# Optimization experiments

Hardware: AMD Instinct MI355X
Metric: run time of the kernel (lower is better)

## Reference

```python
import jax, jax.numpy as jnp
import numpy as np

B=8; C=2; H=256; W=64; PH=4; PW=4; HP=H//PH; WP=W//PW; N=HP*WP
HID=1024; NH=16; HD=HID//NH; DEPTH=8; FFN=int(int(HID*4)*2/3); TDIM=256; OUT=PH*PW*C
EPS=1e-6


def _rmsnorm(x, w):
    return x * jax.lax.rsqrt(jnp.mean(x*x, -1, keepdims=True) + EPS) * w


def _modulate(x, shift, scale):
    return x * (1.0 + scale[:, None, :]) + shift[:, None, :]


def _rotate_half(x):
    x1 = x[..., 0::2]
    x2 = x[..., 1::2]
    return jnp.stack([-x2, x1], axis=-1).reshape(x.shape)


def _rope_tables():
    # 2D axial RoPE (EVA VisionRotaryEmbeddingFast style), dim per axis = HD//2
    dim = HD // 2
    freqs = 1.0 / (10000.0 ** (np.arange(0, dim, 2, dtype=np.float32) / dim))
    fh = np.repeat(np.outer(np.arange(HP, dtype=np.float32), freqs), 2, axis=-1)  # [HP,dim]
    fw = np.repeat(np.outer(np.arange(WP, dtype=np.float32), freqs), 2, axis=-1)  # [WP,dim]
    f = np.concatenate([np.broadcast_to(fh[:, None, :], (HP, WP, dim)),
                        np.broadcast_to(fw[None, :, :], (HP, WP, dim))], -1).reshape(N, HD)
    return jnp.asarray(np.cos(f)), jnp.asarray(np.sin(f))


def _sincos_1d(dim, pos):
    omega = np.arange(dim // 2, dtype=np.float32) / (dim / 2.0)
    omega = 1.0 / 10000.0 ** omega
    out = np.einsum('n,d->nd', pos.reshape(-1).astype(np.float32), omega)
    return np.concatenate([np.sin(out), np.cos(out)], -1)


def _pos_embed():
    gw, gh = np.meshgrid(np.arange(WP), np.arange(HP))  # row-major (HP, WP) grids
    emb = np.concatenate([_sincos_1d(HID // 2, gw), _sincos_1d(HID // 2, gh)], -1)
    return jnp.asarray(emb, dtype=jnp.float32)  # [N, HID]


_COS, _SIN = _rope_tables()
_POS = _pos_embed()


def _timestep_emb(t):
    half = TDIM // 2
    freqs = jnp.exp(-jnp.log(jnp.float32(10000.0)) * jnp.arange(half, dtype=jnp.float32) / half)
    args = t[:, None] * freqs[None]
    return jnp.concatenate([jnp.cos(args), jnp.sin(args)], -1)


def setup_inputs() -> dict:
    key = jax.random.key(0)
    ks = iter(jax.random.split(key, 16))
    def w(shape, s=0.02):
        return jax.random.normal(next(ks), shape, dtype=jnp.float32) * s
    return {
        'x': jax.random.normal(next(ks), (B, C, H, W), dtype=jnp.float32),
        't': jax.random.uniform(next(ks), (B,), dtype=jnp.float32) * 1000.0,
        'patch_w': w((HID, C, PH, PW)), 'patch_b': jnp.zeros((HID,), jnp.float32),
        't_w': w((HID, TDIM)), 't_b': jnp.zeros((HID,), jnp.float32),
        'norm1_w': jnp.ones((DEPTH, HID), jnp.float32),
        'qkv_w': w((DEPTH, 3 * HID, HID)), 'qkv_b': jnp.zeros((DEPTH, 3 * HID), jnp.float32),
        'qn_w': jnp.ones((DEPTH, HD), jnp.float32), 'kn_w': jnp.ones((DEPTH, HD), jnp.float32),
        'proj_w': w((DEPTH, HID, HID)), 'proj_b': jnp.zeros((DEPTH, HID), jnp.float32),
        'norm2_w': jnp.ones((DEPTH, HID), jnp.float32),
        'w12_w': w((DEPTH, 2 * FFN, HID)), 'w12_b': jnp.zeros((DEPTH, 2 * FFN), jnp.float32),
        'w3_w': w((DEPTH, HID, FFN)), 'w3_b': jnp.zeros((DEPTH, HID), jnp.float32),
        'ada_w': w((DEPTH, 6 * HID, HID)), 'ada_b': jnp.zeros((DEPTH, 6 * HID), jnp.float32),
        'fnorm_w': jnp.ones((HID,), jnp.float32),
        'flin_w': w((OUT, HID)), 'flin_b': jnp.zeros((OUT,), jnp.float32),
        'fada_w': w((2 * HID, HID)), 'fada_b': jnp.zeros((2 * HID,), jnp.float32),
    }


def reference(x, t, patch_w, patch_b, t_w, t_b, norm1_w, qkv_w, qkv_b, qn_w, kn_w,
              proj_w, proj_b, norm2_w, w12_w, w12_b, w3_w, w3_b, ada_w, ada_b,
              fnorm_w, flin_w, flin_b, fada_w, fada_b):
    # timestep embedding -> c : [B, HID]
    c = _timestep_emb(t) @ t_w.T + t_b
    cs = jax.nn.silu(c)
    # patch embed (conv stride==kernel == patchify + matmul)
    xp = x.reshape(B, C, HP, PH, WP, PW)
    h = jnp.einsum('bchpwq,ocpq->bhwo', xp, patch_w).reshape(B, N, HID) + patch_b
    h = h + _POS[None]
    scale = 1.0 / np.sqrt(HD)
    for d in range(DEPTH):
        ada = cs @ ada_w[d].T + ada_b[d]
        sm, scm, gm, sp, scp, gp = jnp.split(ada, 6, axis=-1)
        hn = _modulate(_rmsnorm(h, norm1_w[d]), sm, scm)
        qkv = (hn @ qkv_w[d].T + qkv_b[d]).reshape(B, N, 3, NH, HD).transpose(2, 0, 3, 1, 4)
        q, k, v = qkv[0], qkv[1], qkv[2]  # [B, NH, N, HD]
        q = _rmsnorm(q, qn_w[d]) 
        k = _rmsnorm(k, kn_w[d])
        q = q * _COS + _rotate_half(q) * _SIN
        k = k * _COS + _rotate_half(k) * _SIN
        attn = jax.nn.softmax(jnp.einsum('bhqd,bhkd->bhqk', q, k) * scale, axis=-1)
        o = jnp.einsum('bhqk,bhkd->bqhd', attn, v).reshape(B, N, HID)
        o = o @ proj_w[d].T + proj_b[d]
        h = h + gm[:, None, :] * o
        hn = _modulate(_rmsnorm(h, norm2_w[d]), sp, scp)
        x12 = hn @ w12_w[d].T + w12_b[d]
        x1, x2 = jnp.split(x12, 2, axis=-1)
        h = h + gp[:, None, :] * ((jax.nn.silu(x1) * x2) @ w3_w[d].T + w3_b[d])
    fsh, fsc = jnp.split(cs @ fada_w.T + fada_b, 2, axis=-1)
    h = _modulate(_rmsnorm(h, fnorm_w), fsh, fsc) @ flin_w.T + flin_b  # [B, N, OUT]
    y = h.reshape(B, HP, WP, PH, PW, C)
    return jnp.einsum('nhwpqc->nchpwq', y).reshape(B, C, H, W)
```

## Files before the change

kernel.cpp:

```cpp
#include <hip/hip_runtime.h>
#include <stdint.h>

typedef __bf16 bf16;
typedef __attribute__((ext_vector_type(8))) __bf16 bf16x8;
typedef __attribute__((ext_vector_type(4))) float floatx4;

#define NTOK   1024
#define TOKS   8192
#define HID_   1024
#define FFN_   2730
#define FFNP   2816
#define X12N   5460

#define EPI_BF16  0
#define EPI_QKV   1
#define EPI_RESID 2

__global__ __launch_bounds__(256) void conv_bf16(const float* __restrict__ in, bf16* __restrict__ out, int n)
{
    const int i = (blockIdx.x * 256 + threadIdx.x) * 4;
    if (i >= n) return;
    const float4 v = *(const float4*)(in + i);
    out[i + 0] = (bf16)v.x; out[i + 1] = (bf16)v.y;
    out[i + 2] = (bf16)v.z; out[i + 3] = (bf16)v.w;
}

__global__ void conv_pad_w3(const float* __restrict__ w3, bf16* __restrict__ w3p)
{
    const int kk = blockIdx.x * 256 + threadIdx.x;
    const int row = blockIdx.y;
    if (kk >= FFNP) return;
    w3p[(size_t)row * FFNP + kk] = (kk < FFN_) ? (bf16)w3[(size_t)row * FFN_ + kk] : (bf16)0.f;
}

#define GLL(src, dst) __builtin_amdgcn_global_load_lds( \
    (const __attribute__((address_space(1))) void*)(src), \
    (__attribute__((address_space(3))) void*)(dst), 16, 0, 0)

#define STAGE_A(bufi, hi, tile) GLL(pA[hi] + (size_t)(tile) * 64, As + (bufi) * 16384 + ((hi) * 512 + t) * 8)
#define STAGE_B(bufi, hi, tile) GLL(pB[hi] + (size_t)(tile) * 64, Bs + (bufi) * 16384 + ((hi) * 512 + t) * 8)

#define LOADA(bufi, qm) { _Pragma("unroll") for (int mf = 0; mf < 4; mf++) { \
    a[mf][0] = *(const bf16x8*)(As + (bufi) * 16384 + (qm) * 8192 + arow64 + mf * 1024 + swz0); \
    a[mf][1] = *(const bf16x8*)(As + (bufi) * 16384 + (qm) * 8192 + arow64 + mf * 1024 + swz1); } }

#define LOADB(bufi, qn) { _Pragma("unroll") for (int nf = 0; nf < 2; nf++) { \
    b[nf][0] = *(const bf16x8*)(Bs + (bufi) * 16384 + (qn) * 8192 + brow64 + nf * 1024 + swz0); \
    b[nf][1] = *(const bf16x8*)(Bs + (bufi) * 16384 + (qn) * 8192 + brow64 + nf * 1024 + swz1); } }

#define MM(qm, qn) { _Pragma("unroll") for (int mf = 0; mf < 4; mf++) \
    _Pragma("unroll") for (int nf = 0; nf < 2; nf++) { \
    acc[qm][qn][mf][nf] = __builtin_amdgcn_mfma_f32_16x16x32_bf16(a[mf][0], b[nf][0], acc[qm][qn][mf][nf], 0, 0, 0); \
    acc[qm][qn][mf][nf] = __builtin_amdgcn_mfma_f32_16x16x32_bf16(a[mf][1], b[nf][1], acc[qm][qn][mf][nf], 0, 0, 0); } }

#define PHTAIL(...) { __builtin_amdgcn_s_barrier(); \
    asm volatile("s_waitcnt lgkmcnt(0)" ::: "memory"); \
    __builtin_amdgcn_sched_barrier(0); \
    __builtin_amdgcn_s_setprio(1); __VA_ARGS__; __builtin_amdgcn_s_setprio(0); \
    __builtin_amdgcn_s_barrier(); }

__global__ __launch_bounds__(512, 2) void gemm256(
    const bf16* __restrict__ A, const bf16* __restrict__ Bm, const float* __restrict__ bias,
    int K, int Nreal, int epi,
    bf16* __restrict__ outb, int ldo,
    bf16* __restrict__ qo, bf16* __restrict__ ko, bf16* __restrict__ vo,
    float* __restrict__ hres, const float* __restrict__ gate, int gstride)
{
    __shared__ __align__(16) bf16 As[2 * 16384];
    __shared__ __align__(16) bf16 Bs[2 * 16384];
    const int t = threadIdx.x;

    const int gx = gridDim.x;
    int wg = blockIdx.y * gx + blockIdx.x;
    {
        const int nwg = gx * gridDim.y;
        const int q8 = nwg >> 3, r8 = nwg & 7;
        const int xcd = wg & 7, pos = wg >> 3;
        wg = (xcd < r8 ? xcd * (q8 + 1) : r8 * (q8 + 1) + (xcd - r8) * q8) + pos;
    }
    const int M0 = (wg / gx) * 256, N0 = (wg % gx) * 256;
    const int Nlast = Nreal - 1;

    const int lane = t & 63, w = t >> 6;
    const int wm = w >> 2, wn = w & 3;
    const int quad = lane >> 4, r16 = lane & 15;

    const int rS = t >> 3;
    const int cswS = (t & 7) ^ (rS & 7);
    const bf16* pA[4]; const bf16* pB[4];
    #pragma unroll
    for (int hi = 0; hi < 4; hi++) {
        pA[hi] = A + (size_t)(M0 + hi * 64 + rS) * K + cswS * 8;
        int nb = N0 + hi * 64 + rS; if (nb > Nlast) nb = Nlast;
        pB[hi] = Bm + (size_t)nb * K + cswS * 8;
    }

    const int arow64 = (wm * 64 + r16) * 64;
    const int brow64 = (wn * 32 + r16) * 64;
    const int swz0 = ((0 * 4 + quad) ^ (r16 & 7)) * 8;
    const int swz1 = ((1 * 4 + quad) ^ (r16 & 7)) * 8;

    floatx4 acc[2][2][4][2];
    const floatx4 zero = {0.f, 0.f, 0.f, 0.f};
    #pragma unroll
    for (int i0 = 0; i0 < 2; i0++)
        #pragma unroll
        for (int i1 = 0; i1 < 2; i1++)
            #pragma unroll
            for (int i2 = 0; i2 < 4; i2++)
                #pragma unroll
                for (int i3 = 0; i3 < 2; i3++) acc[i0][i1][i2][i3] = zero;
    bf16x8 a[4][2], b[2][2];

    const int NT = K >> 6;
    const int NI = NT >> 1;

    STAGE_A(0, 0, 0); STAGE_A(0, 1, 0);
    STAGE_B(0, 0, 0); STAGE_B(0, 1, 0);
    STAGE_B(0, 2, 0); STAGE_B(0, 3, 0);
    STAGE_A(0, 2, 0); STAGE_A(0, 3, 0);
    STAGE_A(1, 0, 1); STAGE_A(1, 1, 1);
    STAGE_B(1, 0, 1); STAGE_B(1, 1, 1);
    asm volatile("s_waitcnt vmcnt(4)" ::: "memory");
    __builtin_amdgcn_s_barrier();

    for (int it = 0; it < NI; ++it) {
        const bool last = (it == NI - 1);
        const int to = 2 * it + 1, te2 = 2 * it + 2, to2 = 2 * it + 3;
        LOADA(0, 0); LOADB(0, 0);
        STAGE_A(1, 2, to); STAGE_A(1, 3, to);
        PHTAIL(MM(0, 0));
        LOADB(0, 1);
        STAGE_B(1, 2, to); STAGE_B(1, 3, to);
        PHTAIL(MM(0, 1));
        LOADA(0, 1); LOADB(0, 0);
        if (!last) { STAGE_A(0, 0, te2); STAGE_A(0, 1, te2); }
        PHTAIL(MM(1, 0));
        LOADB(0, 1);
        if (!last) { STAGE_B(0, 0, te2); STAGE_B(0, 1, te2);
                     asm volatile("s_waitcnt vmcnt(4)" ::: "memory"); }
        else       { asm volatile("s_waitcnt vmcnt(0)" ::: "memory"); }
        PHTAIL(MM(1, 1));
        LOADA(1, 0); LOADB(1, 0);
        if (!last) { STAGE_A(0, 2, te2); STAGE_A(0, 3, te2); }
        PHTAIL(MM(0, 0));
        LOADB(1, 1);
        if (!last) { STAGE_B(0, 2, te2); STAGE_B(0, 3, te2); }
        PHTAIL(MM(0, 1));
        LOADA(1, 1); LOADB(1, 0);
        if (!last) { STAGE_A(1, 0, to2); STAGE_A(1, 1, to2); }
        PHTAIL(MM(1, 0));
        LOADB(1, 1);
        if (!last) { STAGE_B(1, 0, to2); STAGE_B(1, 1, to2);
                     asm volatile("s_waitcnt vmcnt(4)" ::: "memory"); }
        PHTAIL(MM(1, 1));
    }

    #pragma unroll
    for (int qm = 0; qm < 2; qm++)
    #pragma unroll
    for (int mf = 0; mf < 4; mf++) {
        const int rbase = M0 + qm * 128 + wm * 64 + mf * 16 + quad * 4;
        #pragma unroll
        for (int qn = 0; qn < 2; qn++)
        #pragma unroll
        for (int nf = 0; nf < 2; nf++) {
            const int col = N0 + qn * 128 + wn * 32 + nf * 16 + r16;
            if (col >= Nreal) continue;
            const float bv = bias[col];
            const floatx4 av = acc[qm][qn][mf][nf];
            if (epi == EPI_BF16) {
                #pragma unroll
                for (int rr = 0; rr < 4; rr++)
                    outb[(size_t)(rbase + rr) * ldo + col] = (bf16)(av[rr] + bv);
            } else if (epi == EPI_QKV) {
                const int s = col >> 10, hh = (col >> 6) & 15, dd = col & 63;
                #pragma unroll
                for (int rr = 0; rr < 4; rr++) {
                    const int row = rbase + rr;
                    const int bb = row >> 10, n = row & 1023;
                    const float vv = av[rr] + bv;
                    if (s == 0)      qo[((size_t)(bb * 16 + hh) * 1024 + n) * 64 + dd] = (bf16)vv;
                    else if (s == 1) ko[((size_t)(bb * 16 + hh) * 1024 + n) * 64 + dd] = (bf16)vv;
                    else             vo[((size_t)(bb * 16 + hh) * 64 + dd) * 1024 + n] = (bf16)vv;
                }
            } else {
                #pragma unroll
                for (int rr = 0; rr < 4; rr++) {
                    const int row = rbase + rr;
                    const int bb = row >> 10;
                    hres[(size_t)row * 1024 + col] += gate[(size_t)bb * gstride + col] * (av[rr] + bv);
                }
            }
        }
    }
}

__global__ __launch_bounds__(256) void small_gemm(
    const float* __restrict__ Aws, const float* __restrict__ t_in,
    const float* __restrict__ W, const float* __restrict__ bias,
    float* __restrict__ out, int N, int K, int mode, int dosilu)
{
    const int w = threadIdx.x >> 6, lane = threadIdx.x & 63;
    const int col = blockIdx.x * 4 + w;
    float acc[8];
    #pragma unroll
    for (int bb = 0; bb < 8; bb++) acc[bb] = 0.f;
    float tb[8];
    if (mode == 1) {
        #pragma unroll
        for (int bb = 0; bb < 8; bb++) tb[bb] = t_in[bb];
    }
    for (int kk = lane; kk < K; kk += 64) {
        const float wv = W[(size_t)col * K + kk];
        if (mode == 1) {
            const float f = __expf(-(float)(kk & 127) * (9.21034037198f / 128.f));
            #pragma unroll
            for (int bb = 0; bb < 8; bb++) {
                const float arg = tb[bb] * f;
                const float e = (kk < 128) ? cosf(arg) : sinf(arg);
                acc[bb] += e * wv;
            }
        } else {
            #pragma unroll
            for (int bb = 0; bb < 8; bb++) acc[bb] += Aws[(size_t)bb * 1024 + kk] * wv;
        }
    }
    #pragma unroll
    for (int bb = 0; bb < 8; bb++) {
        float v2 = acc[bb];
        #pragma unroll
        for (int off = 32; off; off >>= 1) v2 += __shfl_xor(v2, off, 64);
        acc[bb] = v2;
    }
    if (lane == 0) {
        const float bv = bias[col];
        #pragma unroll
        for (int bb = 0; bb < 8; bb++) {
            float vv = acc[bb] + bv;
            if (dosilu) vv = vv / (1.f + __expf(-vv));
            out[(size_t)bb * N + col] = vv;
        }
    }
}

__global__ __launch_bounds__(256) void patch_embed(
    const float* __restrict__ x, const float* __restrict__ pw, const float* __restrict__ pb,
    float* __restrict__ h)
{
    __shared__ float xs[32];
    const int row = blockIdx.x, t = threadIdx.x;
    const int b = row >> 10, n = row & 1023;
    const int hp = n >> 4, wp = n & 15;
    if (t < 32) {
        const int c = t >> 4, ph = (t >> 2) & 3, pq = t & 3;
        xs[t] = x[((size_t)(b * 2 + c) * 256 + hp * 4 + ph) * 64 + wp * 4 + pq];
    }
    __syncthreads();
    #pragma unroll
    for (int rep = 0; rep < 4; rep++) {
        const int o = t + rep * 256;
        const float* wrow = pw + (size_t)o * 32;
        float acc = pb[o];
        #pragma unroll
        for (int e = 0; e < 32; e++) acc += xs[e] * wrow[e];
        const int seg = o >> 8, oo = o & 255;
        const float om = __expf(-(float)oo * (9.21034037198f / 256.f));
        const float pos = (seg < 2) ? (float)wp : (float)hp;
        const float arg = pos * om;
        const float pe = ((seg & 1) == 0) ? sinf(arg) : cosf(arg);
        h[(size_t)row * 1024 + o] = acc + pe;
    }
}

__global__ __launch_bounds__(256) void norm_mod(
    const float* __restrict__ h, const float* __restrict__ w,
    const float* __restrict__ ada, int sh_off, int sc_off, int stride,
    bf16* __restrict__ out)
{
    __shared__ float red[4];
    const int row = blockIdx.x, t = threadIdx.x;
    const int b = row >> 10;
    const float4 xv = ((const float4*)(h + (size_t)row * 1024))[t];
    float ss = xv.x * xv.x + xv.y * xv.y + xv.z * xv.z + xv.w * xv.w;
    #pragma unroll
    for (int off = 32; off; off >>= 1) ss += __shfl_xor(ss, off, 64);
    if ((t & 63) == 0) red[t >> 6] = ss;
    __syncthreads();
    const float total = red[0] + red[1] + red[2] + red[3];
    const float rms = rsqrtf(total * (1.f / 1024.f) + 1e-6f);
    const float* sh = ada + (size_t)b * stride + sh_off;
    const float* sc = ada + (size_t)b * stride + sc_off;
    const float vals[4] = {xv.x, xv.y, xv.z, xv.w};
    #pragma unroll
    for (int e = 0; e < 4; e++) {
        const int c2 = t * 4 + e;
        const float vv = vals[e] * rms * w[c2] * (1.f + sc[c2]) + sh[c2];
        out[(size_t)row * 1024 + c2] = (bf16)vv;
    }
}

__global__ __launch_bounds__(256) void rope_qk(
    bf16* __restrict__ q, bf16* __restrict__ k,
    const float* __restrict__ qw, const float* __restrict__ kw)
{
    const int n = blockIdx.x * 4 + (threadIdx.x >> 6);
    const int bh = blockIdx.y, d = threadIdx.x & 63;
    const size_t idx = ((size_t)bh * 1024 + n) * 64 + d;
    const float qv = (float)q[idx], kv = (float)k[idx];
    float sq = qv * qv, sk = kv * kv;
    #pragma unroll
    for (int off = 32; off; off >>= 1) { sq += __shfl_xor(sq, off, 64); sk += __shfl_xor(sk, off, 64); }
    const float rq = rsqrtf(sq * (1.f / 64.f) + 1e-6f);
    const float rk = rsqrtf(sk * (1.f / 64.f) + 1e-6f);
    const float qn = qv * rq * qw[d];
    const float kn = kv * rk * kw[d];
    const int j = (d & 31) >> 1;
    const float freq = __expf(-(float)j * (9.21034037198f / 16.f));
    const float pos = (d < 32) ? (float)(n >> 4) : (float)(n & 15);
    const float ang = pos * freq;
    const float cv = cosf(ang), sv = sinf(ang);
    const float qp = __shfl_xor(qn, 1, 64);
    const float kp = __shfl_xor(kn, 1, 64);
    const float qo = qn * cv + ((d & 1) ? qp : -qp) * sv;
    const float ko = kn * cv + ((d & 1) ? kp : -kp) * sv;
    q[idx] = (bf16)qo;
    k[idx] = (bf16)ko;
}

__global__ __launch_bounds__(256) void attn_kernel(
    const bf16* __restrict__ q, const bf16* __restrict__ k, const bf16* __restrict__ v,
    bf16* __restrict__ o)
{
    __shared__ __align__(16) bf16 Qs[2 * 64 * 32];
    __shared__ __align__(16) bf16 Ks[2 * 64 * 32];
    __shared__ __align__(16) bf16 Vt[2 * 64 * 32];
    __shared__ __align__(16) bf16 Pw[4 * 16 * 80];
    const int t = threadIdx.x;
    const int l = t & 63, wq = t >> 6;
    const int quad = l >> 4, r16 = l & 15;
    const int qt = blockIdx.x, bh = blockIdx.y;
    const int b = bh >> 4, hh = bh & 15;

    #pragma unroll
    for (int m = 0; m < 2; m++) {
        const bf16* g = q + ((size_t)bh * 1024 + qt * 64 + wq * 16 + (l >> 2)) * 64 + m * 32 + (l & 3) * 8;
        __builtin_amdgcn_global_load_lds((const __attribute__((address_space(1))) void*)g,
            (__attribute__((address_space(3))) void*)(Qs + m * 2048 + wq * 16 * 32 + l * 8), 16, 0, 0);
    }
    __syncthreads();
    bf16x8 afq[2];
    #pragma unroll
    for (int h2 = 0; h2 < 2; h2++)
        afq[h2] = *(const bf16x8*)(Qs + h2 * 2048 + (wq * 16 + r16) * 32 + quad * 8);

    float m_r[4], l_r[4];
    floatx4 oacc[4];
    const floatx4 zero = {0.f, 0.f, 0.f, 0.f};
    #pragma unroll
    for (int rr = 0; rr < 4; rr++) { m_r[rr] = -1e30f; l_r[rr] = 0.f; }
    #pragma unroll
    for (int jd = 0; jd < 4; jd++) oacc[jd] = zero;

    bf16* Pme = Pw + wq * 16 * 80;

    for (int kt = 0; kt < 16; kt++) {
        __syncthreads();
        #pragma unroll
        for (int m = 0; m < 2; m++) {
            const bf16* gk = k + ((size_t)bh * 1024 + kt * 64 + wq * 16 + (l >> 2)) * 64 + m * 32 + (l & 3) * 8;
            __builtin_amdgcn_global_load_lds((const __attribute__((address_space(1))) void*)gk,
                (__attribute__((address_space(3))) void*)(Ks + m * 2048 + wq * 16 * 32 + l * 8), 16, 0, 0);
            const bf16* gv = v + ((size_t)bh * 64 + wq * 16 + (l >> 2)) * 1024 + kt * 64 + m * 32 + (l & 3) * 8;
            __builtin_amdgcn_global_load_lds((const __attribute__((address_space(1))) void*)gv,
                (__attribute__((address_space(3))) void*)(Vt + m * 2048 + wq * 16 * 32 + l * 8), 16, 0, 0);
        }
        __syncthreads();

        floatx4 s[4];
        #pragma unroll
        for (int j = 0; j < 4; j++) {
            bf16x8 b0 = *(const bf16x8*)(Ks + 0 * 2048 + (j * 16 + r16) * 32 + quad * 8);
            bf16x8 b1 = *(const bf16x8*)(Ks + 1 * 2048 + (j * 16 + r16) * 32 + quad * 8);
            s[j] = __builtin_amdgcn_mfma_f32_16x16x32_bf16(afq[0], b0, zero, 0, 0, 0);
            s[j] = __builtin_amdgcn_mfma_f32_16x16x32_bf16(afq[1], b1, s[j], 0, 0, 0);
        }
        float alpha[4];
        #pragma unroll
        for (int rr = 0; rr < 4; rr++) {
            float mx = fmaxf(fmaxf(s[0][rr], s[1][rr]), fmaxf(s[2][rr], s[3][rr])) * 0.125f;
            #pragma unroll
            for (int off2 = 1; off2 < 16; off2 <<= 1) mx = fmaxf(mx, __shfl_xor(mx, off2, 64));
            const float mn = fmaxf(m_r[rr], mx);
            float ps = 0.f;
            #pragma unroll
            for (int j = 0; j < 4; j++) {
                const float e = __expf(s[j][rr] * 0.125f - mn);
                s[j][rr] = e; ps += e;
            }
            #pragma unroll
            for (int off2 = 1; off2 < 16; off2 <<= 1) ps += __shfl_xor(ps, off2, 64);
            alpha[rr] = __expf(m_r[rr] - mn);
            l_r[rr] = l_r[rr] * alpha[rr] + ps;
            m_r[rr] = mn;
        }
        #pragma unroll
        for (int j = 0; j < 4; j++)
            #pragma unroll
            for (int rr = 0; rr < 4; rr++)
                Pme[(quad * 4 + rr) * 80 + j * 16 + r16] = (bf16)s[j][rr];
        __asm__ volatile("s_waitcnt lgkmcnt(0)" ::: "memory");
        bf16x8 afp[2];
        #pragma unroll
        for (int st = 0; st < 2; st++)
            afp[st] = *(const bf16x8*)(Pme + r16 * 80 + st * 32 + quad * 8);
        #pragma unroll
        for (int jd = 0; jd < 4; jd++)
            #pragma unroll
            for (int rr = 0; rr < 4; rr++) oacc[jd][rr] *= alpha[rr];
        #pragma unroll
        for (int jd = 0; jd < 4; jd++) {
            bf16x8 b0 = *(const bf16x8*)(Vt + 0 * 2048 + (jd * 16 + r16) * 32 + quad * 8);
            bf16x8 b1 = *(const bf16x8*)(Vt + 1 * 2048 + (jd * 16 + r16) * 32 + quad * 8);
            oacc[jd] = __builtin_amdgcn_mfma_f32_16x16x32_bf16(afp[0], b0, oacc[jd], 0, 0, 0);
            oacc[jd] = __builtin_amdgcn_mfma_f32_16x16x32_bf16(afp[1], b1, oacc[jd], 0, 0, 0);
        }
    }
    #pragma unroll
    for (int rr = 0; rr < 4; rr++) {
        const float inv = 1.f / l_r[rr];
        const size_t base = ((size_t)b * 1024 + qt * 64 + wq * 16 + quad * 4 + rr) * 1024 + hh * 64;
        #pragma unroll
        for (int jd = 0; jd < 4; jd++)
            o[base + jd * 16 + r16] = (bf16)(oacc[jd][rr] * inv);
    }
}

__global__ void swiglu_kernel(const bf16* __restrict__ x12, bf16* __restrict__ g)
{
    const int kk = blockIdx.x * 256 + threadIdx.x;
    const int row = blockIdx.y;
    if (kk >= FFNP) return;
    float gv = 0.f;
    if (kk < FFN_) {
        const float a  = (float)x12[(size_t)row * X12N + kk];
        const float b2 = (float)x12[(size_t)row * X12N + FFN_ + kk];
        gv = a * b2 / (1.f + __expf(-a));
    }
    g[(size_t)row * FFNP + kk] = (bf16)gv;
}

__global__ __launch_bounds__(256) void final_head(
    const bf16* __restrict__ hn, const float* __restrict__ fw, const float* __restrict__ fb,
    float* __restrict__ out)
{
    __shared__ float hs[1024];
    const int row = blockIdx.x, t = threadIdx.x;
    #pragma unroll
    for (int r = 0; r < 4; r++) hs[t + r * 256] = (float)hn[(size_t)row * 1024 + t + r * 256];
    __syncthreads();
    const int o = t >> 3, s = t & 7;
    float acc = 0.f;
    const float* wr = fw + (size_t)o * 1024 + s * 128;
    const float* hb = hs + s * 128;
    for (int e = 0; e < 128; e++) acc += hb[e] * wr[e];
    #pragma unroll
    for (int off = 1; off < 8; off <<= 1) acc += __shfl_xor(acc, off, 64);
    if (s == 0) {
        acc += fb[o];
        const int b = row >> 10, n = row & 1023;
        const int hp = n >> 4, wp = n & 15;
        const int ph = o >> 3, pw = (o >> 1) & 3, c = o & 1;
        out[((size_t)(b * 2 + c) * 256 + hp * 4 + ph) * 64 + wp * 4 + pw] = acc;
    }
}

extern "C" void kernel_launch(void* const* d_in, const int* in_sizes, int n_in,
                              void* d_out, int out_size, void* d_ws, size_t ws_size,
                              hipStream_t stream)
{
    const float* x       = (const float*)d_in[0];
    const float* t_in    = (const float*)d_in[1];
    const float* patch_w = (const float*)d_in[2];
    const float* patch_b = (const float*)d_in[3];
    const float* t_w     = (const float*)d_in[4];
    const float* t_b     = (const float*)d_in[5];
    const float* norm1_w = (const float*)d_in[6];
    const float* qkv_w   = (const float*)d_in[7];
    const float* qkv_b   = (const float*)d_in[8];
    const float* qn_w    = (const float*)d_in[9];
    const float* kn_w    = (const float*)d_in[10];
    const float* proj_w  = (const float*)d_in[11];
    const float* proj_b  = (const float*)d_in[12];
    const float* norm2_w = (const float*)d_in[13];
    const float* w12_w   = (const float*)d_in[14];
    const float* w12_b   = (const float*)d_in[15];
    const float* w3_w    = (const float*)d_in[16];
    const float* w3_b    = (const float*)d_in[17];
    const float* ada_w   = (const float*)d_in[18];
    const float* ada_b   = (const float*)d_in[19];
    const float* fnorm_w = (const float*)d_in[20];
    const float* flin_w  = (const float*)d_in[21];
    const float* flin_b  = (const float*)d_in[22];
    const float* fada_w  = (const float*)d_in[23];
    const float* fada_b  = (const float*)d_in[24];

    char* ws = (char*)d_ws;
    size_t off = 0;
    auto alloc = [&](size_t nbytes) { char* p = ws + off; off += (nbytes + 255) & ~(size_t)255; return p; };
    float* h     = (float*)alloc((size_t)TOKS * 1024 * 4);
    float* cs    = (float*)alloc(8 * 1024 * 4);
    float* ada   = (float*)alloc(8 * 6144 * 4);
    float* fada  = (float*)alloc(8 * 2048 * 4);
    bf16*  hn    = (bf16*)alloc((size_t)TOKS * 1024 * 2);
    char*  U1    =         alloc((size_t)TOKS * X12N * 2);
    bf16*  qb    = (bf16*)U1;
    bf16*  kb    = qb + (size_t)TOKS * 1024;
    bf16*  vb    = kb + (size_t)TOKS * 1024;
    bf16*  ob    = vb + (size_t)TOKS * 1024;
    bf16*  x12   = (bf16*)U1;
    bf16*  g     = (bf16*)alloc((size_t)TOKS * FFNP * 2);
    bf16*  wqkvb = (bf16*)alloc((size_t)3072 * 1024 * 2);
    bf16*  wprjb = (bf16*)alloc((size_t)1024 * 1024 * 2);
    bf16*  w12b  = (bf16*)alloc((size_t)X12N * 1024 * 2);
    bf16*  w3p   = (bf16*)alloc((size_t)1024 * FFNP * 2);
    (void)ws_size; (void)in_sizes; (void)n_in; (void)out_size;

    small_gemm<<<dim3(1024 / 4), 256, 0, stream>>>(nullptr, t_in, t_w, t_b, cs, 1024, 256, 1, 1);
    patch_embed<<<dim3(TOKS), 256, 0, stream>>>(x, patch_w, patch_b, h);

    for (int d = 0; d < 8; d++) {
        small_gemm<<<dim3(6144 / 4), 256, 0, stream>>>(cs, nullptr,
            ada_w + (size_t)d * 6144 * 1024, ada_b + (size_t)d * 6144, ada, 6144, 1024, 0, 0);
        norm_mod<<<dim3(TOKS), 256, 0, stream>>>(h, norm1_w + (size_t)d * 1024, ada, 0, 1024, 6144, hn);
        conv_bf16<<<dim3(3072 * 1024 / 4 / 256), 256, 0, stream>>>(qkv_w + (size_t)d * 3072 * 1024, wqkvb, 3072 * 1024);
        gemm256<<<dim3(3072 / 256, 32), 512, 0, stream>>>(hn,
            wqkvb, qkv_b + (size_t)d * 3072, 1024, 3072, EPI_QKV,
            nullptr, 0, qb, kb, vb, nullptr, nullptr, 0);
        rope_qk<<<dim3(256, 128), 256, 0, stream>>>(qb, kb, qn_w + (size_t)d * 64, kn_w + (size_t)d * 64);
        attn_kernel<<<dim3(16, 128), 256, 0, stream>>>(qb, kb, vb, ob);
        conv_bf16<<<dim3(1024 * 1024 / 4 / 256), 256, 0, stream>>>(proj_w + (size_t)d * 1024 * 1024, wprjb, 1024 * 1024);
        gemm256<<<dim3(1024 / 256, 32), 512, 0, stream>>>(ob,
            wprjb, proj_b + (size_t)d * 1024, 1024, 1024, EPI_RESID,
            nullptr, 0, nullptr, nullptr, nullptr, h, ada + 2048, 6144);
        norm_mod<<<dim3(TOKS), 256, 0, stream>>>(h, norm2_w + (size_t)d * 1024, ada, 3072, 4096, 6144, hn);
        conv_bf16<<<dim3(X12N * 1024 / 4 / 256), 256, 0, stream>>>(w12_w + (size_t)d * X12N * 1024, w12b, X12N * 1024);
        gemm256<<<dim3((X12N + 255) / 256, 32), 512, 0, stream>>>(hn,
            w12b, w12_b + (size_t)d * X12N, 1024, X12N, EPI_BF16,
            x12, X12N, nullptr, nullptr, nullptr, nullptr, nullptr, 0);
        swiglu_kernel<<<dim3(FFNP / 256, TOKS), 256, 0, stream>>>(x12, g);
        conv_pad_w3<<<dim3(FFNP / 256, 1024), 256, 0, stream>>>(w3_w + (size_t)d * 1024 * FFN_, w3p);
        gemm256<<<dim3(1024 / 256, 32), 512, 0, stream>>>(g,
            w3p, w3_b + (size_t)d * 1024, FFNP, 1024, EPI_RESID,
            nullptr, 0, nullptr, nullptr, nullptr, h, ada + 5120, 6144);
    }

    small_gemm<<<dim3(2048 / 4), 256, 0, stream>>>(cs, nullptr, fada_w, fada_b, fada, 2048, 1024, 0, 0);
    norm_mod<<<dim3(TOKS), 256, 0, stream>>>(h, fnorm_w, fada, 0, 1024, 2048, hn);
    final_head<<<dim3(TOKS), 256, 0, stream>>>(hn, flin_w, flin_b, (float*)d_out);
}
```

Before: 5.558 ms.

## Add 128x256 triple-buffered GEMM for small-N layers and reuse B fragments

Adds a gemm128 kernel with 128-row M tiles and a three-stage LDS pipeline. It is used for the QKV, proj and w3 GEMMs, whose smaller grids (128 or 384 workgroups with 256-row tiles) underfill the 256 CUs; halving the M tile doubles the workgroup count. In gemm256, B fragments are kept in two register sets so each B quarter is loaded from LDS once per k-step instead of twice. The cost is lower per-workgroup arithmetic intensity and more register pressure, which could lower occupancy.

Result: faster. 4.996 ms (-10.1%).

```diff
diff --git a/kernel.cpp b/kernel.cpp
--- a/kernel.cpp
+++ b/kernel.cpp
@@ -37,27 +37,32 @@
     (const __attribute__((address_space(1))) void*)(src), \
     (__attribute__((address_space(3))) void*)(dst), 16, 0, 0)
 
-#define STAGE_A(bufi, hi, tile) GLL(pA[hi] + (size_t)(tile) * 64, As + (bufi) * 16384 + ((hi) * 512 + t) * 8)
-#define STAGE_B(bufi, hi, tile) GLL(pB[hi] + (size_t)(tile) * 64, Bs + (bufi) * 16384 + ((hi) * 512 + t) * 8)
-
-#define LOADA(bufi, qm) { _Pragma("unroll") for (int mf = 0; mf < 4; mf++) { \
-    a[mf][0] = *(const bf16x8*)(As + (bufi) * 16384 + (qm) * 8192 + arow64 + mf * 1024 + swz0); \
-    a[mf][1] = *(const bf16x8*)(As + (bufi) * 16384 + (qm) * 8192 + arow64 + mf * 1024 + swz1); } }
-
-#define LOADB(bufi, qn) { _Pragma("unroll") for (int nf = 0; nf < 2; nf++) { \
-    b[nf][0] = *(const bf16x8*)(Bs + (bufi) * 16384 + (qn) * 8192 + brow64 + nf * 1024 + swz0); \
-    b[nf][1] = *(const bf16x8*)(Bs + (bufi) * 16384 + (qn) * 8192 + brow64 + nf * 1024 + swz1); } }
-
-#define MM(qm, qn) { _Pragma("unroll") for (int mf = 0; mf < 4; mf++) \
-    _Pragma("unroll") for (int nf = 0; nf < 2; nf++) { \
-    acc[qm][qn][mf][nf] = __builtin_amdgcn_mfma_f32_16x16x32_bf16(a[mf][0], b[nf][0], acc[qm][qn][mf][nf], 0, 0, 0); \
-    acc[qm][qn][mf][nf] = __builtin_amdgcn_mfma_f32_16x16x32_bf16(a[mf][1], b[nf][1], acc[qm][qn][mf][nf], 0, 0, 0); } }
-
 #define PHTAIL(...) { __builtin_amdgcn_s_barrier(); \
     asm volatile("s_waitcnt lgkmcnt(0)" ::: "memory"); \
     __builtin_amdgcn_sched_barrier(0); \
     __builtin_amdgcn_s_setprio(1); __VA_ARGS__; __builtin_amdgcn_s_setprio(0); \
     __builtin_amdgcn_s_barrier(); }
+
+#define XCD_SWZ(wg, nwg) { \
+    const int q8 = (nwg) >> 3, r8 = (nwg) & 7; \
+    const int xcd = (wg) & 7, pos = (wg) >> 3; \
+    wg = (xcd < r8 ? xcd * (q8 + 1) : r8 * (q8 + 1) + (xcd - r8) * q8) + pos; }
+
+#define STAGE_A(bufi, hi, tile) GLL(pA[hi] + (size_t)(tile) * 64, As + (bufi) * 16384 + ((hi) * 512 + t) * 8)
+#define STAGE_B(bufi, hi, tile) GLL(pB[hi] + (size_t)(tile) * 64, Bs + (bufi) * 16384 + ((hi) * 512 + t) * 8)
+
+#define LOADA(bufi, qm) { _Pragma("unroll") for (int mf = 0; mf < 4; mf++) { \
+    a[mf][0] = *(const bf16x8*)(As + (bufi) * 16384 + (qm) * 8192 + arow64 + mf * 1024 + swz0); \
+    a[mf][1] = *(const bf16x8*)(As + (bufi) * 16384 + (qm) * 8192 + arow64 + mf * 1024 + swz1); } }
+
+#define LOADB(bufi, qn, breg) { _Pragma("unroll") for (int nf = 0; nf < 2; nf++) { \
+    breg[nf][0] = *(const bf16x8*)(Bs + (bufi) * 16384 + (qn) * 8192 + brow64 + nf * 1024 + swz0); \
+    breg[nf][1] = *(const bf16x8*)(Bs + (bufi) * 16384 + (qn) * 8192 + brow64 + nf * 1024 + swz1); } }
+
+#define MM2(qm, qn, breg) { _Pragma("unroll") for (int mf = 0; mf < 4; mf++) \
+    _Pragma("unroll") for (int nf = 0; nf < 2; nf++) { \
+    acc[qm][qn][mf][nf] = __builtin_amdgcn_mfma_f32_16x16x32_bf16(a[mf][0], breg[nf][0], acc[qm][qn][mf][nf], 0, 0, 0); \
+    acc[qm][qn][mf][nf] = __builtin_amdgcn_mfma_f32_16x16x32_bf16(a[mf][1], breg[nf][1], acc[qm][qn][mf][nf], 0, 0, 0); } }
 
 __global__ __launch_bounds__(512, 2) void gemm256(
     const bf16* __restrict__ A, const bf16* __restrict__ Bm, const float* __restrict__ bias,
@@ -72,12 +77,7 @@
 
     const int gx = gridDim.x;
     int wg = blockIdx.y * gx + blockIdx.x;
-    {
-        const int nwg = gx * gridDim.y;
-        const int q8 = nwg >> 3, r8 = nwg & 7;
-        const int xcd = wg & 7, pos = wg >> 3;
-        wg = (xcd < r8 ? xcd * (q8 + 1) : r8 * (q8 + 1) + (xcd - r8) * q8) + pos;
-    }
+    { const int nwg = gx * gridDim.y; XCD_SWZ(wg, nwg); }
     const int M0 = (wg / gx) * 256, N0 = (wg % gx) * 256;
     const int Nlast = Nreal - 1;
 
@@ -110,7 +110,7 @@
             for (int i2 = 0; i2 < 4; i2++)
                 #pragma unroll
                 for (int i3 = 0; i3 < 2; i3++) acc[i0][i1][i2][i3] = zero;
-    bf16x8 a[4][2], b[2][2];
+    bf16x8 a[4][2], b0[2][2], b1[2][2];
 
     const int NT = K >> 6;
     const int NI = NT >> 1;
@@ -127,33 +127,31 @@
     for (int it = 0; it < NI; ++it) {
         const bool last = (it == NI - 1);
         const int to = 2 * it + 1, te2 = 2 * it + 2, to2 = 2 * it + 3;
-        LOADA(0, 0); LOADB(0, 0);
+        LOADA(0, 0); LOADB(0, 0, b0);
         STAGE_A(1, 2, to); STAGE_A(1, 3, to);
-        PHTAIL(MM(0, 0));
-        LOADB(0, 1);
+        PHTAIL(MM2(0, 0, b0));
+        LOADB(0, 1, b1);
         STAGE_B(1, 2, to); STAGE_B(1, 3, to);
-        PHTAIL(MM(0, 1));
-        LOADA(0, 1); LOADB(0, 0);
+        PHTAIL(MM2(0, 1, b1));
+        LOADA(0, 1);
         if (!last) { STAGE_A(0, 0, te2); STAGE_A(0, 1, te2); }
-        PHTAIL(MM(1, 0));
-        LOADB(0, 1);
+        PHTAIL(MM2(1, 0, b0));
         if (!last) { STAGE_B(0, 0, te2); STAGE_B(0, 1, te2);
                      asm volatile("s_waitcnt vmcnt(4)" ::: "memory"); }
         else       { asm volatile("s_waitcnt vmcnt(0)" ::: "memory"); }
-        PHTAIL(MM(1, 1));
-        LOADA(1, 0); LOADB(1, 0);
+        PHTAIL(MM2(1, 1, b1));
+        LOADA(1, 0); LOADB(1, 0, b0);
         if (!last) { STAGE_A(0, 2, te2); STAGE_A(0, 3, te2); }
-        PHTAIL(MM(0, 0));
-        LOADB(1, 1);
+        PHTAIL(MM2(0, 0, b0));
+        LOADB(1, 1, b1);
         if (!last) { STAGE_B(0, 2, te2); STAGE_B(0, 3, te2); }
-        PHTAIL(MM(0, 1));
-        LOADA(1, 1); LOADB(1, 0);
+        PHTAIL(MM2(0, 1, b1));
+        LOADA(1, 1);
         if (!last) { STAGE_A(1, 0, to2); STAGE_A(1, 1, to2); }
-        PHTAIL(MM(1, 0));
-        LOADB(1, 1);
+        PHTAIL(MM2(1, 0, b0));
         if (!last) { STAGE_B(1, 0, to2); STAGE_B(1, 1, to2);
                      asm volatile("s_waitcnt vmcnt(4)" ::: "memory"); }
-        PHTAIL(MM(1, 1));
+        PHTAIL(MM2(1, 1, b1));
     }
 
     #pragma unroll
@@ -196,6 +194,133 @@
     }
 }
 
+#define STA1(bufi, hi, tile) GLL(pA[hi] + (size_t)(tile) * 64, As + (bufi) * 8192  + ((hi) * 512 + t) * 8)
+#define STB1(bufi, hi, tile) GLL(pB[hi] + (size_t)(tile) * 64, Bs + (bufi) * 16384 + ((hi) * 512 + t) * 8)
+
+#define LA1(bufi) { _Pragma("unroll") for (int mf = 0; mf < 4; mf++) { \
+    a[mf][0] = *(const bf16x8*)(As + (bufi) * 8192 + arow64 + mf * 1024 + swz0); \
+    a[mf][1] = *(const bf16x8*)(As + (bufi) * 8192 + arow64 + mf * 1024 + swz1); } }
+
+#define LB1(bufi, qn, breg) { _Pragma("unroll") for (int nf = 0; nf < 2; nf++) { \
+    breg[nf][0] = *(const bf16x8*)(Bs + (bufi) * 16384 + (qn) * 8192 + brow64 + nf * 1024 + swz0); \
+    breg[nf][1] = *(const bf16x8*)(Bs + (bufi) * 16384 + (qn) * 8192 + brow64 + nf * 1024 + swz1); } }
+
+#define MM1(qn, breg) { _Pragma("unroll") for (int mf = 0; mf < 4; mf++) \
+    _Pragma("unroll") for (int nf = 0; nf < 2; nf++) { \
+    acc[qn][mf][nf] = __builtin_amdgcn_mfma_f32_16x16x32_bf16(a[mf][0], breg[nf][0], acc[qn][mf][nf], 0, 0, 0); \
+    acc[qn][mf][nf] = __builtin_amdgcn_mfma_f32_16x16x32_bf16(a[mf][1], breg[nf][1], acc[qn][mf][nf], 0, 0, 0); } }
+
+__global__ __launch_bounds__(512, 2) void gemm128(
+    const bf16* __restrict__ A, const bf16* __restrict__ Bm, const float* __restrict__ bias,
+    int K, int Nreal, int epi,
+    bf16* __restrict__ outb, int ldo,
+    bf16* __restrict__ qo, bf16* __restrict__ ko, bf16* __restrict__ vo,
+    float* __restrict__ hres, const float* __restrict__ gate, int gstride)
+{
+    __shared__ __align__(16) bf16 As[3 * 8192];
+    __shared__ __align__(16) bf16 Bs[3 * 16384];
+    const int t = threadIdx.x;
+
+    const int gx = gridDim.x;
+    int wg = blockIdx.y * gx + blockIdx.x;
+    { const int nwg = gx * gridDim.y; XCD_SWZ(wg, nwg); }
+    const int M0 = (wg / gx) * 128, N0 = (wg % gx) * 256;
+    const int Nlast = Nreal - 1;
+
+    const int lane = t & 63, w = t >> 6;
+    const int wm = w >> 2, wn = w & 3;
+    const int quad = lane >> 4, r16 = lane & 15;
+
+    const int rS = t >> 3;
+    const int cswS = (t & 7) ^ (rS & 7);
+    const bf16* pA[2]; const bf16* pB[4];
+    #pragma unroll
+    for (int hi = 0; hi < 2; hi++)
+        pA[hi] = A + (size_t)(M0 + hi * 64 + rS) * K + cswS * 8;
+    #pragma unroll
+    for (int hi = 0; hi < 4; hi++) {
+        int nb = N0 + hi * 64 + rS; if (nb > Nlast) nb = Nlast;
+        pB[hi] = Bm + (size_t)nb * K + cswS * 8;
+    }
+
+    const int arow64 = (wm * 64 + r16) * 64;
+    const int brow64 = (wn * 32 + r16) * 64;
+    const int swz0 = ((0 * 4 + quad) ^ (r16 & 7)) * 8;
+    const int swz1 = ((1 * 4 + quad) ^ (r16 & 7)) * 8;
+
+    floatx4 acc[2][4][2];
+    const floatx4 zero = {0.f, 0.f, 0.f, 0.f};
+    #pragma unroll
+    for (int i0 = 0; i0 < 2; i0++)
+        #pragma unroll
+        for (int i1 = 0; i1 < 4; i1++)
+            #pragma unroll
+            for (int i2 = 0; i2 < 2; i2++) acc[i0][i1][i2] = zero;
+    bf16x8 a[4][2], b0[2][2], b1[2][2];
+
+    const int NT = K >> 6;
+
+    STA1(0, 0, 0); STA1(0, 1, 0);
+    STB1(0, 0, 0); STB1(0, 1, 0); STB1(0, 2, 0); STB1(0, 3, 0);
+    STA1(1, 0, 1); STA1(1, 1, 1);
+    STB1(1, 0, 1); STB1(1, 1, 1); STB1(1, 2, 1); STB1(1, 3, 1);
+    asm volatile("s_waitcnt vmcnt(6)" ::: "memory");
+    __builtin_amdgcn_s_barrier();
+
+    int bufR = 0;
+    for (int tt = 0; tt < NT; ++tt) {
+        const int ts = tt + 2;
+        const int bufS = (bufR == 0) ? 2 : bufR - 1;
+        const bool st = (ts < NT);
+        LA1(bufR); LB1(bufR, 0, b0);
+        if (st) { STA1(bufS, 0, ts); STA1(bufS, 1, ts); STB1(bufS, 0, ts); }
+        PHTAIL(MM1(0, b0));
+        LB1(bufR, 1, b1);
+        if (st) { STB1(bufS, 1, ts); STB1(bufS, 2, ts); STB1(bufS, 3, ts); }
+        if (tt < NT - 2)       { asm volatile("s_waitcnt vmcnt(6)" ::: "memory"); }
+        else if (tt == NT - 2) { asm volatile("s_waitcnt vmcnt(0)" ::: "memory"); }
+        PHTAIL(MM1(1, b1));
+        bufR = (bufR == 2) ? 0 : bufR + 1;
+    }
+
+    #pragma unroll
+    for (int mf = 0; mf < 4; mf++) {
+        const int rbase = M0 + wm * 64 + mf * 16 + quad * 4;
+        #pragma unroll
+        for (int qn = 0; qn < 2; qn++)
+        #pragma unroll
+        for (int nf = 0; nf < 2; nf++) {
+            const int col = N0 + qn * 128 + wn * 32 + nf * 16 + r16;
+            if (col >= Nreal) continue;
+            const float bv = bias[col];
+            const floatx4 av = acc[qn][mf][nf];
+            if (epi == EPI_BF16) {
+                #pragma unroll
+                for (int rr = 0; rr < 4; rr++)
+                    outb[(size_t)(rbase + rr) * ldo + col] = (bf16)(av[rr] + bv);
+            } else if (epi == EPI_QKV) {
+                const int s = col >> 10, hh = (col >> 6) & 15, dd = col & 63;
+                #pragma unroll
+                for (int rr = 0; rr < 4; rr++) {
+                    const int row = rbase + rr;
+                    const int bb = row >> 10, n = row & 1023;
+                    const float vv = av[rr] + bv;
+                    if (s == 0)      qo[((size_t)(bb * 16 + hh) * 1024 + n) * 64 + dd] = (bf16)vv;
+                    else if (s == 1) ko[((size_t)(bb * 16 + hh) * 1024 + n) * 64 + dd] = (bf16)vv;
+                    else             vo[((size_t)(bb * 16 + hh) * 64 + dd) * 1024 + n] = (bf16)vv;
+                }
+            } else {
+                #pragma unroll
+                for (int rr = 0; rr < 4; rr++) {
+                    const int row = rbase + rr;
+                    const int bb = row >> 10;
+                    hres[(size_t)row * 1024 + col] += gate[(size_t)bb * gstride + col] * (av[rr] + bv);
+                }
+            }
+        }
+    }
+}
+
 __global__ __launch_bounds__(256) void small_gemm(
     const float* __restrict__ Aws, const float* __restrict__ t_in,
     const float* __restrict__ W, const float* __restrict__ bias,
@@ -380,10 +505,10 @@
         floatx4 s[4];
         #pragma unroll
         for (int j = 0; j < 4; j++) {
-            bf16x8 b0 = *(const bf16x8*)(Ks + 0 * 2048 + (j * 16 + r16) * 32 + quad * 8);
-            bf16x8 b1 = *(const bf16x8*)(Ks + 1 * 2048 + (j * 16 + r16) * 32 + quad * 8);
-            s[j] = __builtin_amdgcn_mfma_f32_16x16x32_bf16(afq[0], b0, zero, 0, 0, 0);
-            s[j] = __builtin_amdgcn_mfma_f32_16x16x32_bf16(afq[1], b1, s[j], 0, 0, 0);
+            bf16x8 k0 = *(const bf16x8*)(Ks + 0 * 2048 + (j * 16 + r16) * 32 + quad * 8);
+            bf16x8 k1 = *(const bf16x8*)(Ks + 1 * 2048 + (j * 16 + r16) * 32 + quad * 8);
+            s[j] = __builtin_amdgcn_mfma_f32_16x16x32_bf16(afq[0], k0, zero, 0, 0, 0);
+            s[j] = __builtin_amdgcn_mfma_f32_16x16x32_bf16(afq[1], k1, s[j], 0, 0, 0);
         }
         float alpha[4];
         #pragma unroll
@@ -420,10 +545,10 @@
             for (int rr = 0; rr < 4; rr++) oacc[jd][rr] *= alpha[rr];
         #pragma unroll
         for (int jd = 0; jd < 4; jd++) {
-            bf16x8 b0 = *(const bf16x8*)(Vt + 0 * 2048 + (jd * 16 + r16) * 32 + quad * 8);
-            bf16x8 b1 = *(const bf16x8*)(Vt + 1 * 2048 + (jd * 16 + r16) * 32 + quad * 8);
-            oacc[jd] = __builtin_amdgcn_mfma_f32_16x16x32_bf16(afp[0], b0, oacc[jd], 0, 0, 0);
-            oacc[jd] = __builtin_amdgcn_mfma_f32_16x16x32_bf16(afp[1], b1, oacc[jd], 0, 0, 0);
+            bf16x8 v0 = *(const bf16x8*)(Vt + 0 * 2048 + (jd * 16 + r16) * 32 + quad * 8);
+            bf16x8 v1 = *(const bf16x8*)(Vt + 1 * 2048 + (jd * 16 + r16) * 32 + quad * 8);
+            oacc[jd] = __builtin_amdgcn_mfma_f32_16x16x32_bf16(afp[0], v0, oacc[jd], 0, 0, 0);
+            oacc[jd] = __builtin_amdgcn_mfma_f32_16x16x32_bf16(afp[1], v1, oacc[jd], 0, 0, 0);
         }
     }
     #pragma unroll
@@ -534,23 +659,23 @@
             ada_w + (size_t)d * 6144 * 1024, ada_b + (size_t)d * 6144, ada, 6144, 1024, 0, 0);
         norm_mod<<<dim3(TOKS), 256, 0, stream>>>(h, norm1_w + (size_t)d * 1024, ada, 0, 1024, 6144, hn);
         conv_bf16<<<dim3(3072 * 1024 / 4 / 256), 256, 0, stream>>>(qkv_w + (size_t)d * 3072 * 1024, wqkvb, 3072 * 1024);
-        gemm256<<<dim3(3072 / 256, 32), 512, 0, stream>>>(hn,
+        gemm128<<<dim3(3072 / 256, TOKS / 128), 512, 0, stream>>>(hn,
             wqkvb, qkv_b + (size_t)d * 3072, 1024, 3072, EPI_QKV,
             nullptr, 0, qb, kb, vb, nullptr, nullptr, 0);
         rope_qk<<<dim3(256, 128), 256, 0, stream>>>(qb, kb, qn_w + (size_t)d * 64, kn_w + (size_t)d * 64);
         attn_kernel<<<dim3(16, 128), 256, 0, stream>>>(qb, kb, vb, ob);
         conv_bf16<<<dim3(1024 * 1024 / 4 / 256), 256, 0, stream>>>(proj_w + (size_t)d * 1024 * 1024, wprjb, 1024 * 1024);
-        gemm256<<<dim3(1024 / 256, 32), 512, 0, stream>>>(ob,
+        gemm128<<<dim3(1024 / 256, TOKS / 128), 512, 0, stream>>>(ob,
             wprjb, proj_b + (size_t)d * 1024, 1024, 1024, EPI_RESID,
             nullptr, 0, nullptr, nullptr, nullptr, h, ada + 2048, 6144);
         norm_mod<<<dim3(TOKS), 256, 0, stream>>>(h, norm2_w + (size_t)d * 1024, ada, 3072, 4096, 6144, hn);
         conv_bf16<<<dim3(X12N * 1024 / 4 / 256), 256, 0, stream>>>(w12_w + (size_t)d * X12N * 1024, w12b, X12N * 1024);
-        gemm256<<<dim3((X12N + 255) / 256, 32), 512, 0, stream>>>(hn,
+        gemm256<<<dim3((X12N + 255) / 256, TOKS / 256), 512, 0, stream>>>(hn,
             w12b, w12_b + (size_t)d * X12N, 1024, X12N, EPI_BF16,
             x12, X12N, nullptr, nullptr, nullptr, nullptr, nullptr, 0);
         swiglu_kernel<<<dim3(FFNP / 256, TOKS), 256, 0, stream>>>(x12, g);
         conv_pad_w3<<<dim3(FFNP / 256, 1024), 256, 0, stream>>>(w3_w + (size_t)d * 1024 * FFN_, w3p);
-        gemm256<<<dim3(1024 / 256, 32), 512, 0, stream>>>(g,
+        gemm128<<<dim3(1024 / 256, TOKS / 128), 512, 0, stream>>>(g,
             w3p, w3_b + (size_t)d * 1024, FFNP, 1024, EPI_RESID,
             nullptr, 0, nullptr, nullptr, nullptr, h, ada + 5120, 6144);
     }
```
